# Kernel optimization log

Measured on AMD Instinct MI355X. Metric: run time of the kernel, lower is better.

## Reference

```python
import jax, jax.numpy as jnp
import numpy as np

K = 9          # neighbors (module default k=9, dilation=1 -> plain top-k)
COUT = 256     # out_channels
BN_EPS = 1e-5


def setup_inputs() -> dict:
    key = jax.random.key(0)
    k1, k2 = jax.random.split(key, 2)
    x = jax.random.normal(k1, (8, 128, 2048, 1), jnp.float32)          # [B,C,N,1]
    W = jax.random.normal(k2, (COUT, 2 * 128), jnp.float32) * 0.05     # 1x1 conv weight [Cout, 2C]
    gamma = jnp.ones((COUT,), jnp.float32)                             # BN affine scale
    beta = jnp.zeros((COUT,), jnp.float32)                             # BN affine shift
    return {"x": x, "W": W, "gamma": gamma, "beta": beta}


def reference(x, W, gamma, beta):
    # x: [B, C, N, 1] channels-first point features
    xt = jnp.transpose(x[..., 0], (0, 2, 1))                           # [B, N, C]
    B, N, C = xt.shape

    # --- dense KNN graph (matrix form): squared euclidean distance, k nearest ---
    sq = jnp.sum(xt * xt, axis=-1)                                     # [B, N]
    dist = sq[:, :, None] - 2.0 * jnp.einsum('bnc,bmc->bnm', xt, xt) + sq[:, None, :]
    _, nn_idx = jax.lax.top_k(-dist, K)                                # [B, N, K] neighbor indices

    # --- EdgeConv gather: x_i = center, x_j = neighbor ---
    x_j = jax.vmap(lambda f, i: f[i])(xt, nn_idx)                      # [B, N, K, C]
    x_i = xt[:, :, None, :]                                            # [B, N, 1, C]
    feat = jnp.concatenate(
        [jnp.broadcast_to(x_i, (B, N, K, C)), x_j - x_i], axis=-1)     # [B, N, K, 2C]

    # --- 1x1 conv (no bias) as GEMM over channel dim ---
    h = jnp.einsum('bnkc,oc->bnko', feat, W)                           # [B, N, K, Cout]

    # --- BatchNorm2d (training-mode batch stats over B,N,K per channel) ---
    mean = jnp.mean(h, axis=(0, 1, 2))
    var = jnp.var(h, axis=(0, 1, 2))
    hn = (h - mean) * jax.lax.rsqrt(var + BN_EPS) * gamma + beta

    # --- ReLU then max over k neighbors ---
    out = jnp.max(jax.nn.relu(hn), axis=2)                             # [B, N, Cout]
    return jnp.transpose(out, (0, 2, 1))                               # [B, Cout, N]
```

## Files before the change

kernel.cpp:

```cpp
#include <hip/hip_runtime.h>
#include <float.h>
#include <math.h>

#define BATCH 8
#define CHN   128
#define NPTS  2048
#define KNN   9
#define NOUT  256
#define TOTCNT (BATCH*NPTS*KNN)

typedef __attribute__((ext_vector_type(8))) short short8;
typedef __attribute__((ext_vector_type(4))) float f32x4;

__device__ __forceinline__ unsigned short f2bf(float f) {
    unsigned int u = __float_as_uint(f);
    unsigned int r = (u + 0x7FFFu + ((u >> 16) & 1u)) >> 16;
    return (unsigned short)r;
}
__device__ __forceinline__ float bf2f(unsigned short h) {
    return __uint_as_float(((unsigned int)h) << 16);
}

__global__ __launch_bounds__(256) void prep_kernel(const float* __restrict__ x,
                                                   const float* __restrict__ W,
                                                   unsigned short* __restrict__ xhi,
                                                   unsigned short* __restrict__ xlo,
                                                   unsigned short* __restrict__ whi,
                                                   unsigned short* __restrict__ wlo,
                                                   float* __restrict__ sqh,
                                                   float* __restrict__ stats) {
    __shared__ float xt[128 * 65];
    __shared__ float psq[256];
    const int b = blockIdx.x, tid = threadIdx.x;
    if (blockIdx.y == 32) {
        stats[b * 512 + tid] = 0.f;
        stats[b * 512 + 256 + tid] = 0.f;
#pragma unroll
        for (int e = 0; e < 32; ++e) {
            int idx = e * 256 + tid;
            int r = b * 64 + (idx >> 7), c = idx & 127;
            float v = (r < 256) ? (W[r * 256 + c] - W[r * 256 + 128 + c])
                                : W[(r - 256) * 256 + 128 + c];
            unsigned short h = f2bf(v);
            float hf = bf2f(h);
            whi[r * 128 + c] = h;
            wlo[r * 128 + c] = f2bf(v - hf);
        }
        return;
    }
    const int n0 = blockIdx.y * 64;
#pragma unroll 4
    for (int p = 0; p < 32; ++p) {
        int c = p * 4 + (tid >> 6), n = tid & 63;
        xt[c * 65 + n] = x[((size_t)b * CHN + c) * NPTS + n0 + n];
    }
    __syncthreads();
    const int n = tid >> 2, cq = tid & 3;
    size_t row = (size_t)(b * NPTS + n0 + n) * CHN;
    float s = 0.f;
#pragma unroll 8
    for (int j = 0; j < 32; ++j) {
        int c = cq * 32 + j;
        float f = xt[c * 65 + n];
        unsigned short h = f2bf(f);
        float hf = bf2f(h);
        unsigned short l = f2bf(f - hf);
        xhi[row + c] = h;
        xlo[row + c] = l;
        s += f * f;
    }
    psq[tid] = s;
    __syncthreads();
    if (tid < 64)
        sqh[b * NPTS + n0 + tid] =
            0.5f * (psq[tid*4] + psq[tid*4+1] + psq[tid*4+2] + psq[tid*4+3]);
}

__global__ __launch_bounds__(256) void knnpq_mfma(const unsigned short* __restrict__ xhi,
                                                  const unsigned short* __restrict__ xlo,
                                                  const float* __restrict__ sqh,
                                                  const unsigned short* __restrict__ whi,
                                                  const unsigned short* __restrict__ wlo,
                                                  float* __restrict__ pd,
                                                  int* __restrict__ pi,
                                                  float* __restrict__ p,
                                                  unsigned short* __restrict__ q) {
    __shared__ __align__(16) unsigned short aS[8192];
    __shared__ __align__(16) float dts[5120];

    const int tid = threadIdx.x;
    const int b  = blockIdx.x;
    const int zr = blockIdx.z;
    const int sub = zr >> 1;
    const int wv = tid >> 6, lane = tid & 63;
    const int quad = lane >> 4, col = lane & 15;
    const int koff = quad * 8;
    const size_t xb = (size_t)b * NPTS * CHN;

    if (zr & 1) {
        const int nt = blockIdx.y >> 2;
        const int ot = ((blockIdx.y & 3) << 2) | sub;
        const int nbase = nt * 256 + wv * 64;
        const int obase = ot * 32;

        f32x4 acc[4][2];
#pragma unroll
        for (int i = 0; i < 4; ++i)
#pragma unroll
            for (int j = 0; j < 2; ++j) acc[i][j] = (f32x4)0.f;

        for (int chk = 0; chk < 4; ++chk) {
            short8 ah[4], al[4];
#pragma unroll
            for (int i = 0; i < 4; ++i) {
                size_t g = xb + (size_t)(nbase + i * 16 + col) * CHN + chk * 32 + koff;
                ah[i] = *(const short8*)&xhi[g];
                al[i] = *(const short8*)&xlo[g];
            }
#pragma unroll
            for (int j = 0; j < 2; ++j) {
                size_t g = (size_t)(obase + j * 16 + col) * CHN + chk * 32 + koff;
                short8 bh = *(const short8*)&whi[g];
                short8 bl = *(const short8*)&wlo[g];
#pragma unroll
                for (int i = 0; i < 4; ++i) {
                    acc[i][j] = __builtin_amdgcn_mfma_f32_16x16x32_bf16(ah[i], bh, acc[i][j], 0, 0, 0);
                    acc[i][j] = __builtin_amdgcn_mfma_f32_16x16x32_bf16(ah[i], bl, acc[i][j], 0, 0, 0);
                    acc[i][j] = __builtin_amdgcn_mfma_f32_16x16x32_bf16(al[i], bh, acc[i][j], 0, 0, 0);
                }
            }
        }
#pragma unroll
        for (int i = 0; i < 4; ++i)
#pragma unroll
            for (int j = 0; j < 2; ++j) {
                int oc = (obase + j * 16 + col) & 255;
#pragma unroll
                for (int r = 0; r < 4; ++r) {
                    int n = nbase + i * 16 + quad * 4 + r;
                    size_t off = (size_t)(b * NPTS + n) * NOUT + oc;
                    if (ot < 8) p[off] = acc[i][j][r];
                    else        q[off] = f2bf(acc[i][j][r]);
                }
            }
        return;
    }

    const int q0 = blockIdx.y * 64, ms = sub;
    const int msbase = ms * 512;
    const int mcol0 = wv * 32;

#pragma unroll
    for (int t = 0; t < 4; ++t) {
        const int row = t * 16 + (tid >> 4);
        const int off = (tid & 15) << 4;
        short8 v = *(const short8*)&xhi[xb + (size_t)(q0 + row) * CHN + (off >> 1)];
        *(short8*)((char*)aS + row * 256 + (off ^ ((row & 7) << 4))) = v;
    }
    __syncthreads();

    float* dtw = &dts[wv * 1280];

    float dl[KNN]; int il[KNN];
#pragma unroll
    for (int k = 0; k < KNN; ++k) { dl[k] = FLT_MAX; il[k] = 0; }

    auto ins = [&](float v, int idx) {
        if (v < dl[KNN - 1]) {
            bool c0b = v < dl[0];
#pragma unroll
            for (int k = KNN - 1; k >= 1; --k) {
                bool sh   = v < dl[k - 1];
                bool here = v < dl[k];
                float nd = sh ? dl[k - 1] : (here ? v : dl[k]);
                int   ni = sh ? il[k - 1] : (here ? idx : il[k]);
                dl[k] = nd; il[k] = ni;
            }
            if (c0b) { dl[0] = v; il[0] = idx; }
        }
    };

    const int sw  = (col & 7) << 4;
    const int q16 = quad << 4;
    const int cb  = col << 8;
    const char* ab = (const char*)aS;
    const unsigned short* albase = xlo + xb + (size_t)(q0 + col) * CHN + koff;

    for (int iter = 0; iter < 4; ++iter) {
        const int mbase = msbase + iter * 128;
        float sm[2];
#pragma unroll
        for (int j = 0; j < 2; ++j)
            sm[j] = sqh[b * NPTS + mbase + mcol0 + j * 16 + col];

        const size_t boff = xb + (size_t)(mbase + mcol0 + col) * CHN + koff;
        const unsigned short* bph = xhi + boff;
        const unsigned short* bpl = xlo + boff;

        f32x4 acc[4][2];
#pragma unroll
        for (int i = 0; i < 4; ++i)
#pragma unroll
            for (int j = 0; j < 2; ++j) acc[i][j] = (f32x4)0.f;

#pragma unroll
        for (int chk = 0; chk < 4; ++chk) {
            const int o = cb + (((chk << 6) + q16) ^ sw);
            short8 ah[4], al[4];
#pragma unroll
            for (int i = 0; i < 4; ++i) {
                ah[i] = *(const short8*)(ab + i * 4096 + o);
                al[i] = *(const short8*)(albase + i * 2048 + chk * 32);
            }
#pragma unroll
            for (int j = 0; j < 2; ++j) {
                short8 bh = *(const short8*)(bph + j * 2048 + chk * 32);
                short8 bl = *(const short8*)(bpl + j * 2048 + chk * 32);
#pragma unroll
                for (int i = 0; i < 4; ++i) {
                    acc[i][j] = __builtin_amdgcn_mfma_f32_16x16x32_bf16(ah[i], bh, acc[i][j], 0, 0, 0);
                    acc[i][j] = __builtin_amdgcn_mfma_f32_16x16x32_bf16(ah[i], bl, acc[i][j], 0, 0, 0);
                    acc[i][j] = __builtin_amdgcn_mfma_f32_16x16x32_bf16(al[i], bh, acc[i][j], 0, 0, 0);
                }
            }
        }

        const int ibase = mbase + mcol0;
#pragma unroll
        for (int j = 0; j < 2; ++j) {
#pragma unroll
            for (int i = 0; i < 4; ++i)
#pragma unroll
                for (int r = 0; r < 4; ++r) {
                    int q_ = i * 16 + quad * 4 + r;
                    dtw[q_ * 20 + col] = sm[j] - acc[i][j][r];
                }
#pragma unroll
            for (int jj = 0; jj < 4; ++jj) {
                float4 v = *(const float4*)&dtw[lane * 20 + jj * 4];
                float mn4 = fminf(fminf(v.x, v.y), fminf(v.z, v.w));
                if (mn4 < dl[KNN - 1]) {
                    int ib = ibase + j * 16 + jj * 4;
                    ins(v.x, ib); ins(v.y, ib + 1); ins(v.z, ib + 2); ins(v.w, ib + 3);
                }
            }
        }
    }

    __syncthreads();
    float* md = dts;
    int*   mi = (int*)(dts + 2304);
#pragma unroll
    for (int k = 0; k < KNN; ++k) {
        md[lane * 36 + wv * 9 + k] = dl[k];
        mi[lane * 36 + wv * 9 + k] = il[k];
    }
    __syncthreads();
    if (tid < 64) {
        int base = tid * 36;
        int p0 = 0, p1 = 0, p2 = 0, p3 = 0;
        size_t ob = ((size_t)(b * NPTS + q0 + tid) * 4 + ms) * KNN;
        for (int k = 0; k < KNN; ++k) {
            float v0 = (p0 < KNN) ? md[base + p0]      : FLT_MAX;
            float v1 = (p1 < KNN) ? md[base + 9 + p1]  : FLT_MAX;
            float v2 = (p2 < KNN) ? md[base + 18 + p2] : FLT_MAX;
            float v3 = (p3 < KNN) ? md[base + 27 + p3] : FLT_MAX;
            float best = v0; int sel = 0;
            if (v1 < best) { best = v1; sel = 1; }
            if (v2 < best) { best = v2; sel = 2; }
            if (v3 < best) { best = v3; sel = 3; }
            int idx;
            if      (sel == 0) { idx = mi[base + p0];      p0++; }
            else if (sel == 1) { idx = mi[base + 9 + p1];  p1++; }
            else if (sel == 2) { idx = mi[base + 18 + p2]; p2++; }
            else               { idx = mi[base + 27 + p3]; p3++; }
            pd[ob + k] = best;
            pi[ob + k] = idx;
        }
    }
}

__global__ __launch_bounds__(512) void stats2_kernel(const float* __restrict__ p,
                                                     const unsigned short* __restrict__ q,
                                                     const float* __restrict__ pd,
                                                     const int* __restrict__ pi,
                                                     float* __restrict__ stats,
                                                     unsigned int* __restrict__ hmm) {
    __shared__ int idx_s[16 * KNN];
    const int b = blockIdx.x, n0 = blockIdx.y * 16;
    const int tid = threadIdx.x;
    const int o = tid & 255, half = tid >> 8;
    if (tid < 16) {
        size_t g = (size_t)(b * NPTS + n0 + tid) * 36;
        const float* d = pd + g;
        const int*   i = pi + g;
        int p0 = 0, p1 = 0, p2 = 0, p3 = 0;
#pragma unroll
        for (int k = 0; k < KNN; ++k) {
            float v0 = (p0 < KNN) ? d[p0]      : FLT_MAX;
            float v1 = (p1 < KNN) ? d[9 + p1]  : FLT_MAX;
            float v2 = (p2 < KNN) ? d[18 + p2] : FLT_MAX;
            float v3 = (p3 < KNN) ? d[27 + p3] : FLT_MAX;
            float best = v0; int sel = 0;
            if (v1 < best) { best = v1; sel = 1; }
            if (v2 < best) { best = v2; sel = 2; }
            if (v3 < best) { best = v3; sel = 3; }
            int idx;
            if      (sel == 0) { idx = i[p0];      p0++; }
            else if (sel == 1) { idx = i[9 + p1];  p1++; }
            else if (sel == 2) { idx = i[18 + p2]; p2++; }
            else               { idx = i[27 + p3]; p3++; }
            idx_s[tid * KNN + k] = idx;
        }
    }
    __syncthreads();
    const unsigned short* qb = q + (size_t)b * NPTS * NOUT + o;
    float s = 0.f, ss = 0.f;
    const int qbase = half * 8;
    for (int qq = 0; qq < 8; qq += 2) {
        const int qi = qbase + qq;
        size_t off0 = (size_t)(b * NPTS + n0 + qi) * NOUT + o;
        size_t off1 = off0 + NOUT;
        float pv0 = p[off0], pv1 = p[off1];
        float h0[KNN], h1[KNN];
#pragma unroll
        for (int k = 0; k < KNN; ++k)
            h0[k] = bf2f(qb[(size_t)idx_s[qi * KNN + k] * NOUT]);
#pragma unroll
        for (int k = 0; k < KNN; ++k)
            h1[k] = bf2f(qb[(size_t)idx_s[(qi + 1) * KNN + k] * NOUT]);
        float mx0 = -FLT_MAX, mn0 = FLT_MAX, mx1 = -FLT_MAX, mn1 = FLT_MAX;
#pragma unroll
        for (int k = 0; k < KNN; ++k) {
            float a = pv0 + h0[k], c = pv1 + h1[k];
            s += a + c; ss += a * a + c * c;
            mx0 = fmaxf(mx0, a); mn0 = fminf(mn0, a);
            mx1 = fmaxf(mx1, c); mn1 = fminf(mn1, c);
        }
        hmm[off0] = ((unsigned int)f2bf(mx0) << 16) | f2bf(mn0);
        hmm[off1] = ((unsigned int)f2bf(mx1) << 16) | f2bf(mn1);
    }
    atomicAdd(&stats[b * 512 + o], s);
    atomicAdd(&stats[b * 512 + NOUT + o], ss);
}

__global__ __launch_bounds__(512) void final_kernel(const unsigned int* __restrict__ hmm,
                                                    const float* __restrict__ stats,
                                                    const float* __restrict__ gamma,
                                                    const float* __restrict__ beta,
                                                    float* __restrict__ out) {
    __shared__ float tr[256 * 17];
    const int b = blockIdx.x, n0 = blockIdx.y * 16;
    const int tid = threadIdx.x;
    const int o = tid & 255, qh = tid >> 8;
    float sum = 0.f, sumsq = 0.f;
#pragma unroll
    for (int i = 0; i < 8; ++i) {
        sum   += stats[i * 512 + o];
        sumsq += stats[i * 512 + NOUT + o];
    }
    const float inv = 1.f / (float)TOTCNT;
    float mean = sum * inv;
    float var  = sumsq * inv - mean * mean;
    float g    = gamma[o] / sqrtf(var + 1e-5f);
    float bet  = beta[o];
    const bool pos = (g >= 0.f);
#pragma unroll
    for (int qq = 0; qq < 8; ++qq) {
        const int qi = qh * 8 + qq;
        size_t off = (size_t)(b * NPTS + n0 + qi) * NOUT + o;
        unsigned int w = hmm[off];
        float v = bf2f(pos ? (unsigned short)(w >> 16) : (unsigned short)(w & 0xFFFFu));
        float hn = (v - mean) * g + bet;
        tr[o * 17 + qi] = fmaxf(hn, 0.f);
    }
    __syncthreads();
    int oo = tid >> 4, qq = tid & 15;
    for (int pass = 0; pass < 8; ++pass) {
        int o_ = pass * 32 + oo;
        out[((size_t)b * NOUT + o_) * NPTS + n0 + qq] = tr[o_ * 17 + qq];
    }
}

extern "C" void kernel_launch(void* const* d_in, const int* in_sizes, int n_in,
                              void* d_out, int out_size, void* d_ws, size_t ws_size,
                              hipStream_t stream) {
    (void)in_sizes; (void)n_in; (void)out_size; (void)ws_size;
    const float* x     = (const float*)d_in[0];
    const float* W     = (const float*)d_in[1];
    const float* gamma = (const float*)d_in[2];
    const float* beta  = (const float*)d_in[3];
    float* out = (float*)d_out;

    char* ws = (char*)d_ws;
    float*          p     = (float*)ws;
    unsigned short* q     = (unsigned short*)(ws + (16u << 20));
    unsigned short* xhi   = (unsigned short*)(ws + (24u << 20));
    unsigned short* xlo   = (unsigned short*)(ws + (28u << 20));
    unsigned int*   hmm   = (unsigned int*)(ws + (32u << 20));
    unsigned short* whi   = (unsigned short*)(ws + (48u << 20));
    unsigned short* wlo   = (unsigned short*)(ws + (48u << 20) + 131072);
    float*          pd    = (float*)(ws + (49u << 20));
    int*            pi    = (int*)  (ws + (52u << 20));
    float*          sqh   = (float*)(ws + (55u << 20));
    float*          stats = (float*)(ws + (55u << 20) + 65536);

    prep_kernel  <<<dim3(8, 33),    256, 0, stream>>>(x, W, xhi, xlo, whi, wlo, sqh, stats);
    knnpq_mfma   <<<dim3(8, 32, 8), 256, 0, stream>>>(xhi, xlo, sqh, whi, wlo, pd, pi, p, q);
    stats2_kernel<<<dim3(8, 128),   512, 0, stream>>>(p, q, pd, pi, stats, hmm);
    final_kernel <<<dim3(8, 128),   512, 0, stream>>>(hmm, stats, gamma, beta, out);
}
```

Baseline: 202.2 us.

## Restructure KNN tile so each wave owns 16 queries with register top-k merge

The KNN distance kernel no longer stages query rows in LDS. Each wave now keeps its own 16 query points in registers and streams all candidate rows from global memory, with MFMA outputs laid out so each lane holds distances for one query directly. The LDS transpose buffer, the block-level syncs and the serial 4-way merge done by one wave are replaced by a cross-lane shuffle merge of the per-quad top-9 lists, plus an occupancy hint of 4 blocks per CU. The trade-off is more global and L2 traffic for candidate rows, since they are no longer reused across waves, and more insert work during the shuffle merge.

```diff
diff --git a/kernel.cpp b/kernel.cpp
--- a/kernel.cpp
+++ b/kernel.cpp
@@ -76,7 +76,7 @@
             0.5f * (psq[tid*4] + psq[tid*4+1] + psq[tid*4+2] + psq[tid*4+3]);
 }
 
-__global__ __launch_bounds__(256) void knnpq_mfma(const unsigned short* __restrict__ xhi,
+__global__ __launch_bounds__(256, 4) void knnpq_mfma(const unsigned short* __restrict__ xhi,
                                                   const unsigned short* __restrict__ xlo,
                                                   const float* __restrict__ sqh,
                                                   const unsigned short* __restrict__ whi,
@@ -85,9 +85,6 @@
                                                   int* __restrict__ pi,
                                                   float* __restrict__ p,
                                                   unsigned short* __restrict__ q) {
-    __shared__ __align__(16) unsigned short aS[8192];
-    __shared__ __align__(16) float dts[5120];
-
     const int tid = threadIdx.x;
     const int b  = blockIdx.x;
     const int zr = blockIdx.z;
@@ -148,18 +145,18 @@
 
     const int q0 = blockIdx.y * 64, ms = sub;
     const int msbase = ms * 512;
-    const int mcol0 = wv * 32;
-
-#pragma unroll
-    for (int t = 0; t < 4; ++t) {
-        const int row = t * 16 + (tid >> 4);
-        const int off = (tid & 15) << 4;
-        short8 v = *(const short8*)&xhi[xb + (size_t)(q0 + row) * CHN + (off >> 1)];
-        *(short8*)((char*)aS + row * 256 + (off ^ ((row & 7) << 4))) = v;
-    }
-    __syncthreads();
-
-    float* dtw = &dts[wv * 1280];
+    const int myq = q0 + wv * 16 + col;
+
+    short8 qh[4], ql[4];
+    {
+        const unsigned short* qrh = xhi + xb + (size_t)myq * CHN + koff;
+        const unsigned short* qrl = xlo + xb + (size_t)myq * CHN + koff;
+#pragma unroll
+        for (int chk = 0; chk < 4; ++chk) {
+            qh[chk] = *(const short8*)(qrh + chk * 32);
+            ql[chk] = *(const short8*)(qrl + chk * 32);
+        }
+    }
 
     float dl[KNN]; int il[KNN];
 #pragma unroll
@@ -179,103 +176,82 @@
             if (c0b) { dl[0] = v; il[0] = idx; }
         }
     };
-
-    const int sw  = (col & 7) << 4;
-    const int q16 = quad << 4;
-    const int cb  = col << 8;
-    const char* ab = (const char*)aS;
-    const unsigned short* albase = xlo + xb + (size_t)(q0 + col) * CHN + koff;
-
-    for (int iter = 0; iter < 4; ++iter) {
-        const int mbase = msbase + iter * 128;
-        float sm[2];
-#pragma unroll
-        for (int j = 0; j < 2; ++j)
-            sm[j] = sqh[b * NPTS + mbase + mcol0 + j * 16 + col];
-
-        const size_t boff = xb + (size_t)(mbase + mcol0 + col) * CHN + koff;
-        const unsigned short* bph = xhi + boff;
-        const unsigned short* bpl = xlo + boff;
-
-        f32x4 acc[4][2];
-#pragma unroll
-        for (int i = 0; i < 4; ++i)
-#pragma unroll
-            for (int j = 0; j < 2; ++j) acc[i][j] = (f32x4)0.f;
+    auto ins2 = [&](float v, int idx) {
+        if ((v < dl[KNN - 1]) || (v == dl[KNN - 1] && idx < il[KNN - 1])) {
+            bool c0b = (v < dl[0]) || (v == dl[0] && idx < il[0]);
+#pragma unroll
+            for (int k = KNN - 1; k >= 1; --k) {
+                bool sh   = (v < dl[k - 1]) || (v == dl[k - 1] && idx < il[k - 1]);
+                bool here = (v < dl[k])     || (v == dl[k]     && idx < il[k]);
+                float nd = sh ? dl[k - 1] : (here ? v : dl[k]);
+                int   ni = sh ? il[k - 1] : (here ? idx : il[k]);
+                dl[k] = nd; il[k] = ni;
+            }
+            if (c0b) { dl[0] = v; il[0] = idx; }
+        }
+    };
+
+    const unsigned short* mbh = xhi + xb + (size_t)(msbase + col) * CHN + koff;
+    const unsigned short* mbl = xlo + xb + (size_t)(msbase + col) * CHN + koff;
+    const float* smb = sqh + b * NPTS + msbase + quad * 4;
+
+    for (int ch = 0; ch < 8; ++ch) {
+        f32x4 acc[4];
+#pragma unroll
+        for (int i = 0; i < 4; ++i) acc[i] = (f32x4)0.f;
 
 #pragma unroll
         for (int chk = 0; chk < 4; ++chk) {
-            const int o = cb + (((chk << 6) + q16) ^ sw);
-            short8 ah[4], al[4];
+            short8 mh[4], ml[4];
 #pragma unroll
             for (int i = 0; i < 4; ++i) {
-                ah[i] = *(const short8*)(ab + i * 4096 + o);
-                al[i] = *(const short8*)(albase + i * 2048 + chk * 32);
-            }
-#pragma unroll
-            for (int j = 0; j < 2; ++j) {
-                short8 bh = *(const short8*)(bph + j * 2048 + chk * 32);
-                short8 bl = *(const short8*)(bpl + j * 2048 + chk * 32);
-#pragma unroll
-                for (int i = 0; i < 4; ++i) {
-                    acc[i][j] = __builtin_amdgcn_mfma_f32_16x16x32_bf16(ah[i], bh, acc[i][j], 0, 0, 0);
-                    acc[i][j] = __builtin_amdgcn_mfma_f32_16x16x32_bf16(ah[i], bl, acc[i][j], 0, 0, 0);
-                    acc[i][j] = __builtin_amdgcn_mfma_f32_16x16x32_bf16(al[i], bh, acc[i][j], 0, 0, 0);
-                }
-            }
-        }
-
-        const int ibase = mbase + mcol0;
-#pragma unroll
-        for (int j = 0; j < 2; ++j) {
-#pragma unroll
-            for (int i = 0; i < 4; ++i)
-#pragma unroll
-                for (int r = 0; r < 4; ++r) {
-                    int q_ = i * 16 + quad * 4 + r;
-                    dtw[q_ * 20 + col] = sm[j] - acc[i][j][r];
-                }
-#pragma unroll
-            for (int jj = 0; jj < 4; ++jj) {
-                float4 v = *(const float4*)&dtw[lane * 20 + jj * 4];
-                float mn4 = fminf(fminf(v.x, v.y), fminf(v.z, v.w));
-                if (mn4 < dl[KNN - 1]) {
-                    int ib = ibase + j * 16 + jj * 4;
-                    ins(v.x, ib); ins(v.y, ib + 1); ins(v.z, ib + 2); ins(v.w, ib + 3);
-                }
-            }
-        }
-    }
-
-    __syncthreads();
-    float* md = dts;
-    int*   mi = (int*)(dts + 2304);
-#pragma unroll
-    for (int k = 0; k < KNN; ++k) {
-        md[lane * 36 + wv * 9 + k] = dl[k];
-        mi[lane * 36 + wv * 9 + k] = il[k];
-    }
-    __syncthreads();
-    if (tid < 64) {
-        int base = tid * 36;
-        int p0 = 0, p1 = 0, p2 = 0, p3 = 0;
-        size_t ob = ((size_t)(b * NPTS + q0 + tid) * 4 + ms) * KNN;
+                const int ro = i * 16 * CHN + chk * 32;
+                mh[i] = *(const short8*)(mbh + ro);
+                ml[i] = *(const short8*)(mbl + ro);
+            }
+#pragma unroll
+            for (int i = 0; i < 4; ++i) {
+                acc[i] = __builtin_amdgcn_mfma_f32_16x16x32_bf16(mh[i], qh[chk], acc[i], 0, 0, 0);
+                acc[i] = __builtin_amdgcn_mfma_f32_16x16x32_bf16(mh[i], ql[chk], acc[i], 0, 0, 0);
+                acc[i] = __builtin_amdgcn_mfma_f32_16x16x32_bf16(ml[i], qh[chk], acc[i], 0, 0, 0);
+            }
+        }
+
+        const int mb0 = ch << 6;
+#pragma unroll
+        for (int i = 0; i < 4; ++i) {
+            float4 sm = *(const float4*)(smb + mb0 + i * 16);
+            float d0 = sm.x - acc[i][0], d1 = sm.y - acc[i][1];
+            float d2 = sm.z - acc[i][2], d3 = sm.w - acc[i][3];
+            float mn4 = fminf(fminf(d0, d1), fminf(d2, d3));
+            if (mn4 < dl[KNN - 1]) {
+                int ib = msbase + mb0 + i * 16 + quad * 4;
+                ins(d0, ib); ins(d1, ib + 1); ins(d2, ib + 2); ins(d3, ib + 3);
+            }
+        }
+        mbh += 64 * CHN;
+        mbl += 64 * CHN;
+    }
+
+#pragma unroll
+    for (int rd = 0; rd < 2; ++rd) {
+        const int xm = 16 << rd;
+        float pv[KNN]; int pix[KNN];
+#pragma unroll
         for (int k = 0; k < KNN; ++k) {
-            float v0 = (p0 < KNN) ? md[base + p0]      : FLT_MAX;
-            float v1 = (p1 < KNN) ? md[base + 9 + p1]  : FLT_MAX;
-            float v2 = (p2 < KNN) ? md[base + 18 + p2] : FLT_MAX;
-            float v3 = (p3 < KNN) ? md[base + 27 + p3] : FLT_MAX;
-            float best = v0; int sel = 0;
-            if (v1 < best) { best = v1; sel = 1; }
-            if (v2 < best) { best = v2; sel = 2; }
-            if (v3 < best) { best = v3; sel = 3; }
-            int idx;
-            if      (sel == 0) { idx = mi[base + p0];      p0++; }
-            else if (sel == 1) { idx = mi[base + 9 + p1];  p1++; }
-            else if (sel == 2) { idx = mi[base + 18 + p2]; p2++; }
-            else               { idx = mi[base + 27 + p3]; p3++; }
-            pd[ob + k] = best;
-            pi[ob + k] = idx;
+            pv[k]  = __shfl_xor(dl[k], xm, 64);
+            pix[k] = __shfl_xor(il[k], xm, 64);
+        }
+#pragma unroll
+        for (int k = 0; k < KNN; ++k) ins2(pv[k], pix[k]);
+    }
+
+    if (quad == 0) {
+        size_t ob = ((size_t)(b * NPTS + myq) * 4 + ms) * KNN;
+#pragma unroll
+        for (int k = 0; k < KNN; ++k) {
+            pd[ob + k] = dl[k];
+            pi[ob + k] = il[k];
         }
     }
 }
```

Measured after the change: 274.7 us. +35.9%, slower.
